# Performance work log

Hardware: AMD Instinct MI355X
Metric: run time of the kernel (lower is better)

Reference implementation:

```python
import jax, jax.numpy as jnp
import numpy as np

N_HEADS = 8
HEAD_DIM = 64


def setup_inputs() -> dict:
    key = jax.random.key(0)
    ks = jax.random.split(key, 5)
    B, L, D = 2, 2048, 512
    Dh = N_HEADS * HEAD_DIM  # 512
    scale_init = 0.02
    return {
        "x": jax.random.normal(ks[0], (B, L, D), dtype=jnp.float32),
        "wq": jax.random.normal(ks[1], (D, Dh), dtype=jnp.float32) * scale_init,
        "wk": jax.random.normal(ks[2], (D, Dh), dtype=jnp.float32) * scale_init,
        "wv": jax.random.normal(ks[3], (D, Dh), dtype=jnp.float32) * scale_init,
        "wo": jax.random.normal(ks[4], (Dh, D), dtype=jnp.float32) * scale_init,
    }


def reference(x, wq, wk, wv, wo):
    B, L, D = x.shape
    H, Dh = N_HEADS, HEAD_DIM
    scale = 1.0 / (Dh ** 0.5)

    q = (x @ wq).reshape(B, L, H, Dh)
    k = (x @ wk).reshape(B, L, H, Dh)
    v = (x @ wv).reshape(B, L, H, Dh)

    # [B, H, L, S] scores; diagonal (token attending to itself) is masked out.
    scores = jnp.einsum('blhe,bshe->bhls', q, k) * scale
    diag = jnp.eye(L, dtype=bool)  # [L, L]
    scores = jnp.where(diag, -jnp.inf, scores)
    attn = jax.nn.softmax(scores, axis=-1)

    out = jnp.einsum('bhls,bshd->blhd', attn, v).reshape(B, L, H * Dh)
    return out @ wo
```

## Files before the change

### kernel.cpp

```cpp
#include <hip/hip_runtime.h>
#include <hip/hip_bf16.h>
#include <math.h>

typedef __bf16 bf16;
typedef __bf16 bf16x8 __attribute__((ext_vector_type(8)));
typedef float f32x4 __attribute__((ext_vector_type(4)));

#define AS1 __attribute__((address_space(1)))
#define AS3 __attribute__((address_space(3)))

__device__ __forceinline__ void gload_lds16(const void* g, void* l) {
  __builtin_amdgcn_global_load_lds((const AS1 void*)g, (AS3 void*)l, 16, 0, 0);
}

__global__ __launch_bounds__(256) void cvt_x_kernel(const float* __restrict__ x,
                                                    bf16* __restrict__ xb) {
  int i = (blockIdx.x * 256 + threadIdx.x) * 8;
  float4 a = *(const float4*)(x + i);
  float4 b = *(const float4*)(x + i + 4);
  bf16x8 o;
  o[0] = (bf16)a.x; o[1] = (bf16)a.y; o[2] = (bf16)a.z; o[3] = (bf16)a.w;
  o[4] = (bf16)b.x; o[5] = (bf16)b.y; o[6] = (bf16)b.z; o[7] = (bf16)b.w;
  *(bf16x8*)(xb + i) = o;
}

__global__ __launch_bounds__(256) void transpose_w_kernel(
    const float* __restrict__ wq, const float* __restrict__ wk,
    const float* __restrict__ wv, const float* __restrict__ wo,
    bf16* __restrict__ wqkv_t, bf16* __restrict__ wo_t) {
  __shared__ float t[64 * 65];
  int ct = blockIdx.x & 31, kt = blockIdx.x >> 5;
  int p = ct >> 3;
  const float* src = (p == 0) ? wq : (p == 1) ? wk : (p == 2) ? wv : wo;
  int c0 = (ct & 7) * 64;
  int k0 = kt * 64;
  int tid = threadIdx.x;
  for (int i = 0; i < 16; ++i) {
    int idx = i * 256 + tid;
    int r = idx >> 6, c = idx & 63;
    t[r * 65 + c] = src[(size_t)(k0 + r) * 512 + c0 + c];
  }
  __syncthreads();
  for (int i = 0; i < 16; ++i) {
    int idx = i * 256 + tid;
    int cc = idx >> 6, kk = idx & 63;
    float v = t[kk * 65 + cc];
    int col = c0 + cc;
    if (p < 3) wqkv_t[(size_t)(p * 512 + col) * 512 + k0 + kk] = (bf16)v;
    else       wo_t[(size_t)col * 512 + k0 + kk] = (bf16)v;
  }
}

template <int MODE, int BM, int BN>
__global__ __launch_bounds__(256) void gemm_kernel(
    const bf16* __restrict__ A, const bf16* __restrict__ Bt,
    float* __restrict__ Cf, bf16* __restrict__ qw, bf16* __restrict__ kw,
    bf16* __restrict__ vtw, int M, int N, int K) {
  __shared__ bf16 ldsA[BM * 64];
  __shared__ bf16 ldsB[BN * 64];
  constexpr int MF = BM / 32;
  constexpr int NF = BN / 32;
  int tid = threadIdx.x;
  int wave = tid >> 6, l = tid & 63;
  int lr = l & 15, lg = l >> 4;
  int nbm = M / BM;
  int bm = blockIdx.x % nbm, bn = blockIdx.x / nbm;
  int wr = wave >> 1, wc = wave & 1;

  f32x4 acc[MF][NF] = {};

  for (int k0 = 0; k0 < K; k0 += 64) {
    #pragma unroll
    for (int i = 0; i < BM * 128 / 4096; ++i) {
      int off = i * 4096 + tid * 16;
      int r = off >> 7, cb = off & 127;
      gload_lds16((const char*)(A + (size_t)(bm * BM + r) * K + k0) + cb,
                  (char*)ldsA + i * 4096 + wave * 1024);
    }
    #pragma unroll
    for (int i = 0; i < BN * 128 / 4096; ++i) {
      int off = i * 4096 + tid * 16;
      int r = off >> 7, cb = off & 127;
      gload_lds16((const char*)(Bt + (size_t)(bn * BN + r) * K + k0) + cb,
                  (char*)ldsB + i * 4096 + wave * 1024);
    }
    __syncthreads();
    #pragma unroll
    for (int ks = 0; ks < 2; ++ks) {
      bf16x8 af[MF], bfr[NF];
      #pragma unroll
      for (int m = 0; m < MF; ++m)
        af[m] = *(const bf16x8*)(ldsA + (wr * (BM / 2) + m * 16 + lr) * 64 + ks * 32 + lg * 8);
      #pragma unroll
      for (int n = 0; n < NF; ++n)
        bfr[n] = *(const bf16x8*)(ldsB + (wc * (BN / 2) + n * 16 + lr) * 64 + ks * 32 + lg * 8);
      #pragma unroll
      for (int m = 0; m < MF; ++m)
        #pragma unroll
        for (int n = 0; n < NF; ++n)
          acc[m][n] = __builtin_amdgcn_mfma_f32_16x16x32_bf16(af[m], bfr[n], acc[m][n], 0, 0, 0);
    }
    __syncthreads();
  }

  #pragma unroll
  for (int m = 0; m < MF; ++m)
    #pragma unroll
    for (int n = 0; n < NF; ++n)
      #pragma unroll
      for (int j = 0; j < 4; ++j) {
        float v = acc[m][n][j];
        int row = bm * BM + wr * (BM / 2) + m * 16 + lg * 4 + j;
        int col = bn * BN + wc * (BN / 2) + n * 16 + lr;
        if (MODE == 1) {
          Cf[(size_t)row * N + col] = v;
        } else {
          int part = col >> 9, cp = col & 511;
          int h = cp >> 6, d = cp & 63;
          int b = row >> 11, lq = row & 2047;
          size_t bh = (size_t)(b * 8 + h);
          if (part == 0)      qw[(bh * 2048 + lq) * 64 + d] = (bf16)(v * 0.18033688f);
          else if (part == 1) kw[(bh * 2048 + lq) * 64 + d] = (bf16)v;
          else                vtw[(bh * 64 + d) * 2048 + lq] = (bf16)v;
        }
      }
}

__global__ __launch_bounds__(512) void attn_kernel(
    const bf16* __restrict__ qw, const bf16* __restrict__ kw,
    const bf16* __restrict__ vtw, bf16* __restrict__ pO0, bf16* __restrict__ pO1,
    float* __restrict__ pL0, float* __restrict__ pL1) {
  __shared__ bf16 ldsK[2][64 * 64];
  __shared__ bf16 ldsV[2][64 * 64];
  __shared__ bf16 ldsP[8][16 * 64];

  int swzb = ((blockIdx.x & 7) << 6) | (blockIdx.x >> 3);
  int qblk = swzb & 15, kv = (swzb >> 4) & 1, bh = swzb >> 5;

  int tid = threadIdx.x, wave = tid >> 6, l = tid & 63;
  int lr = l & 15, lg = l >> 4;
  const bf16* Q  = qw  + (size_t)bh * 2048 * 64;
  const bf16* Kp = kw  + (size_t)bh * 2048 * 64;
  const bf16* Vt = vtw + (size_t)bh * 64 * 2048;
  int q0 = qblk * 128;
  int td = qblk * 2 + (wave >> 2);
  int qrel = (wave & 3) * 16;

  bf16x8 qf[2];
  #pragma unroll
  for (int ks = 0; ks < 2; ++ks)
    qf[ks] = *(const bf16x8*)(Q + (size_t)(q0 + wave * 16 + lr) * 64 + ks * 32 + lg * 8);

  int rowT = tid >> 3;
  int colT = (tid * 16) & 127;
  int swzcol = colT ^ ((rowT & 7) << 4);
  int swzk = rowT * 128 + swzcol;
  size_t vsrc = (size_t)rowT * 4096 + swzcol;

  f32x4 acc_o[4] = {};
  float l_part[4] = {0.f, 0.f, 0.f, 0.f};

  auto stage = [&](int buf, int t) {
    gload_lds16((const char*)Kp + (size_t)t * 8192 + swzk, (char*)ldsK[buf] + wave * 1024);
    gload_lds16((const char*)Vt + (size_t)t * 128 + vsrc,  (char*)ldsV[buf] + wave * 1024);
  };

  int t0 = kv * 16;
  stage(0, t0);

  int rxor = (lr & 7) << 4;

  for (int tt = 0; tt < 16; ++tt) {
    int t = t0 + tt;
    int buf = tt & 1;
    if (tt < 15) {
      stage(buf ^ 1, t + 1);
      asm volatile("s_waitcnt vmcnt(2)" ::: "memory");
    } else {
      asm volatile("s_waitcnt vmcnt(0)" ::: "memory");
    }
    __builtin_amdgcn_s_barrier();
    __builtin_amdgcn_sched_barrier(0);

    f32x4 sa[4] = {};
    __builtin_amdgcn_s_setprio(1);
    #pragma unroll
    for (int ks = 0; ks < 2; ++ks) {
      #pragma unroll
      for (int n = 0; n < 4; ++n) {
        bf16x8 kf = *(const bf16x8*)((const char*)ldsK[buf] + (n * 16 + lr) * 128 +
                                     ((ks * 64 + lg * 16) ^ rxor));
        sa[n] = __builtin_amdgcn_mfma_f32_16x16x32_bf16(qf[ks], kf, sa[n], 0, 0, 0);
      }
    }
    __builtin_amdgcn_s_setprio(0);

    if (t == td) {
      #pragma unroll
      for (int n = 0; n < 4; ++n)
        #pragma unroll
        for (int j = 0; j < 4; ++j)
          if (n * 16 + lr == qrel + lg * 4 + j) sa[n][j] = -INFINITY;
    }

    #pragma unroll
    for (int n = 0; n < 4; ++n)
      #pragma unroll
      for (int j = 0; j < 4; ++j) {
        float p = exp2f(sa[n][j]);
        sa[n][j] = p;
        l_part[j] += p;
      }

    char* P = (char*)ldsP[wave];
    #pragma unroll
    for (int j = 0; j < 4; ++j) {
      int rowP = lg * 4 + j;
      #pragma unroll
      for (int n = 0; n < 4; ++n)
        *(bf16*)(P + rowP * 128 + (((n * 16 + lr) * 2) ^ ((rowP & 7) << 4))) = (bf16)sa[n][j];
    }

    __builtin_amdgcn_s_setprio(1);
    #pragma unroll
    for (int ks = 0; ks < 2; ++ks) {
      bf16x8 pf = *(const bf16x8*)(P + lr * 128 + ((ks * 64 + lg * 16) ^ rxor));
      #pragma unroll
      for (int n = 0; n < 4; ++n) {
        bf16x8 vf = *(const bf16x8*)((const char*)ldsV[buf] + (n * 16 + lr) * 128 +
                                     ((ks * 64 + lg * 16) ^ rxor));
        acc_o[n] = __builtin_amdgcn_mfma_f32_16x16x32_bf16(pf, vf, acc_o[n], 0, 0, 0);
      }
    }
    __builtin_amdgcn_s_setprio(0);
    __builtin_amdgcn_s_barrier();
  }

  #pragma unroll
  for (int j = 0; j < 4; ++j)
    #pragma unroll
    for (int dd = 1; dd < 16; dd <<= 1) l_part[j] += __shfl_xor(l_part[j], dd);

  bf16*  pO = kv ? pO1 : pO0;
  float* pL = kv ? pL1 : pL0;
  #pragma unroll
  for (int j = 0; j < 4; ++j) {
    int gq = q0 + wave * 16 + lg * 4 + j;
    if (lr == 0) pL[(size_t)bh * 2048 + gq] = l_part[j];
    #pragma unroll
    for (int n = 0; n < 4; ++n)
      pO[((size_t)bh * 2048 + gq) * 64 + n * 16 + lr] = (bf16)acc_o[n][j];
  }
}

__global__ __launch_bounds__(256) void combine_kernel(
    const bf16* __restrict__ pO0, const bf16* __restrict__ pO1,
    const float* __restrict__ pL0, const float* __restrict__ pL1,
    bf16* __restrict__ ao) {
  int idx = blockIdx.x * 256 + threadIdx.x;
  int e8 = idx * 8;
  int row = e8 >> 9, col = e8 & 511;
  int b = row >> 11, lq = row & 2047, h = col >> 6, d0 = col & 63;
  size_t bhq = (size_t)(b * 8 + h) * 2048 + lq;
  size_t src = bhq * 64 + d0;
  bf16x8 va = *(const bf16x8*)(pO0 + src);
  bf16x8 vb = *(const bf16x8*)(pO1 + src);
  float inv = 1.f / (pL0[bhq] + pL1[bhq]);
  bf16x8 o;
  #pragma unroll
  for (int i = 0; i < 8; ++i) o[i] = (bf16)(((float)va[i] + (float)vb[i]) * inv);
  *(bf16x8*)(ao + e8) = o;
}

extern "C" void kernel_launch(void* const* d_in, const int* in_sizes, int n_in,
                              void* d_out, int out_size, void* d_ws, size_t ws_size,
                              hipStream_t stream) {
  const float* x  = (const float*)d_in[0];
  const float* wq = (const float*)d_in[1];
  const float* wk = (const float*)d_in[2];
  const float* wv = (const float*)d_in[3];
  const float* wo = (const float*)d_in[4];

  if (ws_size < (24u << 20)) return;

  char* ws = (char*)d_ws;
  bf16* xb     = (bf16*)(ws);
  bf16* wqkv_t = (bf16*)(ws + (4 << 20));
  bf16* wo_t   = (bf16*)(ws + (6 << 20));
  bf16* q_ws   = (bf16*)(ws + (8 << 20));
  bf16* k_ws   = (bf16*)(ws + (12 << 20));
  bf16* vt_ws  = (bf16*)(ws + (16 << 20));
  bf16*  pO0 = (bf16*)(ws);
  float* pL0 = (float*)(ws + (4 << 20));
  float* pL1 = (float*)(ws + (4 << 20) + (128 << 10));
  bf16*  pO1 = (bf16*)(ws + (20 << 20));
  bf16*  ao  = (bf16*)(ws + (8 << 20));

  cvt_x_kernel<<<1024, 256, 0, stream>>>(x, xb);
  transpose_w_kernel<<<256, 256, 0, stream>>>(wq, wk, wv, wo, wqkv_t, wo_t);
  gemm_kernel<0, 64, 128><<<64 * 12, 256, 0, stream>>>(xb, wqkv_t, nullptr, q_ws, k_ws,
                                                       vt_ws, 4096, 1536, 512);
  attn_kernel<<<512, 512, 0, stream>>>(q_ws, k_ws, vt_ws, pO0, pO1, pL0, pL1);
  combine_kernel<<<1024, 256, 0, stream>>>(pO0, pO1, pL0, pL1, ao);
  gemm_kernel<1, 64, 64><<<64 * 8, 256, 0, stream>>>(ao, wo_t, (float*)d_out, nullptr,
                                                     nullptr, nullptr, 4096, 512, 512);
}
```

Before: 80.63 us.

## Double query rows per wave and split KV into four partitions

```diff
diff --git a/kernel.cpp b/kernel.cpp
--- a/kernel.cpp
+++ b/kernel.cpp
@@ -126,30 +126,36 @@
       }
 }
 
-__global__ __launch_bounds__(512) void attn_kernel(
+__global__ __launch_bounds__(512, 4) void attn_kernel(
     const bf16* __restrict__ qw, const bf16* __restrict__ kw,
-    const bf16* __restrict__ vtw, bf16* __restrict__ pO0, bf16* __restrict__ pO1,
-    float* __restrict__ pL0, float* __restrict__ pL1) {
+    const bf16* __restrict__ vtw,
+    bf16* __restrict__ pO0, bf16* __restrict__ pO1,
+    bf16* __restrict__ pO2, bf16* __restrict__ pO3,
+    float* __restrict__ pL0, float* __restrict__ pL1,
+    float* __restrict__ pL2, float* __restrict__ pL3) {
   __shared__ bf16 ldsK[2][64 * 64];
   __shared__ bf16 ldsV[2][64 * 64];
-  __shared__ bf16 ldsP[8][16 * 64];
+  __shared__ bf16 ldsP[8][2][16 * 64];
 
   int swzb = ((blockIdx.x & 7) << 6) | (blockIdx.x >> 3);
-  int qblk = swzb & 15, kv = (swzb >> 4) & 1, bh = swzb >> 5;
+  int qblk = swzb & 7, kv = (swzb >> 3) & 3, bh = swzb >> 5;
 
   int tid = threadIdx.x, wave = tid >> 6, l = tid & 63;
   int lr = l & 15, lg = l >> 4;
   const bf16* Q  = qw  + (size_t)bh * 2048 * 64;
   const bf16* Kp = kw  + (size_t)bh * 2048 * 64;
   const bf16* Vt = vtw + (size_t)bh * 64 * 2048;
-  int q0 = qblk * 128;
-  int td = qblk * 2 + (wave >> 2);
-  int qrel = (wave & 3) * 16;
-
-  bf16x8 qf[2];
-  #pragma unroll
-  for (int ks = 0; ks < 2; ++ks)
-    qf[ks] = *(const bf16x8*)(Q + (size_t)(q0 + wave * 16 + lr) * 64 + ks * 32 + lg * 8);
+  int q0 = qblk * 256;
+  int td = qblk * 4 + (wave >> 1);
+  int qrelA = (wave & 1) * 32;
+  int qrelB = qrelA + 16;
+
+  bf16x8 qfA[2], qfB[2];
+  #pragma unroll
+  for (int ks = 0; ks < 2; ++ks) {
+    qfA[ks] = *(const bf16x8*)(Q + (size_t)(q0 + wave * 32 + lr) * 64 + ks * 32 + lg * 8);
+    qfB[ks] = *(const bf16x8*)(Q + (size_t)(q0 + wave * 32 + 16 + lr) * 64 + ks * 32 + lg * 8);
+  }
 
   int rowT = tid >> 3;
   int colT = (tid * 16) & 127;
@@ -157,23 +163,23 @@
   int swzk = rowT * 128 + swzcol;
   size_t vsrc = (size_t)rowT * 4096 + swzcol;
 
-  f32x4 acc_o[4] = {};
-  float l_part[4] = {0.f, 0.f, 0.f, 0.f};
+  f32x4 accA[4] = {}, accB[4] = {};
+  float lA[4] = {0.f, 0.f, 0.f, 0.f}, lB[4] = {0.f, 0.f, 0.f, 0.f};
 
   auto stage = [&](int buf, int t) {
     gload_lds16((const char*)Kp + (size_t)t * 8192 + swzk, (char*)ldsK[buf] + wave * 1024);
     gload_lds16((const char*)Vt + (size_t)t * 128 + vsrc,  (char*)ldsV[buf] + wave * 1024);
   };
 
-  int t0 = kv * 16;
+  int t0 = kv * 8;
   stage(0, t0);
 
   int rxor = (lr & 7) << 4;
 
-  for (int tt = 0; tt < 16; ++tt) {
+  for (int tt = 0; tt < 8; ++tt) {
     int t = t0 + tt;
     int buf = tt & 1;
-    if (tt < 15) {
+    if (tt < 7) {
       stage(buf ^ 1, t + 1);
       asm volatile("s_waitcnt vmcnt(2)" ::: "memory");
     } else {
@@ -182,7 +188,7 @@
     __builtin_amdgcn_s_barrier();
     __builtin_amdgcn_sched_barrier(0);
 
-    f32x4 sa[4] = {};
+    f32x4 saA[4] = {}, saB[4] = {};
     __builtin_amdgcn_s_setprio(1);
     #pragma unroll
     for (int ks = 0; ks < 2; ++ks) {
@@ -190,7 +196,8 @@
       for (int n = 0; n < 4; ++n) {
         bf16x8 kf = *(const bf16x8*)((const char*)ldsK[buf] + (n * 16 + lr) * 128 +
                                      ((ks * 64 + lg * 16) ^ rxor));
-        sa[n] = __builtin_amdgcn_mfma_f32_16x16x32_bf16(qf[ks], kf, sa[n], 0, 0, 0);
+        saA[n] = __builtin_amdgcn_mfma_f32_16x16x32_bf16(qfA[ks], kf, saA[n], 0, 0, 0);
+        saB[n] = __builtin_amdgcn_mfma_f32_16x16x32_bf16(qfB[ks], kf, saB[n], 0, 0, 0);
       }
     }
     __builtin_amdgcn_s_setprio(0);
@@ -199,37 +206,39 @@
       #pragma unroll
       for (int n = 0; n < 4; ++n)
         #pragma unroll
-        for (int j = 0; j < 4; ++j)
-          if (n * 16 + lr == qrel + lg * 4 + j) sa[n][j] = -INFINITY;
-    }
-
+        for (int j = 0; j < 4; ++j) {
+          if (n * 16 + lr == qrelA + lg * 4 + j) saA[n][j] = -INFINITY;
+          if (n * 16 + lr == qrelB + lg * 4 + j) saB[n][j] = -INFINITY;
+        }
+    }
+
+    char* PA = (char*)ldsP[wave][0];
+    char* PB = (char*)ldsP[wave][1];
     #pragma unroll
     for (int n = 0; n < 4; ++n)
       #pragma unroll
       for (int j = 0; j < 4; ++j) {
-        float p = exp2f(sa[n][j]);
-        sa[n][j] = p;
-        l_part[j] += p;
+        int rowP = lg * 4 + j;
+        int cswz = ((n * 16 + lr) * 2) ^ ((rowP & 7) << 4);
+        float pA = exp2f(saA[n][j]);
+        lA[j] += pA;
+        *(bf16*)(PA + rowP * 128 + cswz) = (bf16)pA;
+        float pB = exp2f(saB[n][j]);
+        lB[j] += pB;
+        *(bf16*)(PB + rowP * 128 + cswz) = (bf16)pB;
       }
 
-    char* P = (char*)ldsP[wave];
-    #pragma unroll
-    for (int j = 0; j < 4; ++j) {
-      int rowP = lg * 4 + j;
-      #pragma unroll
-      for (int n = 0; n < 4; ++n)
-        *(bf16*)(P + rowP * 128 + (((n * 16 + lr) * 2) ^ ((rowP & 7) << 4))) = (bf16)sa[n][j];
-    }
-
     __builtin_amdgcn_s_setprio(1);
     #pragma unroll
     for (int ks = 0; ks < 2; ++ks) {
-      bf16x8 pf = *(const bf16x8*)(P + lr * 128 + ((ks * 64 + lg * 16) ^ rxor));
+      bf16x8 pfA = *(const bf16x8*)(PA + lr * 128 + ((ks * 64 + lg * 16) ^ rxor));
+      bf16x8 pfB = *(const bf16x8*)(PB + lr * 128 + ((ks * 64 + lg * 16) ^ rxor));
       #pragma unroll
       for (int n = 0; n < 4; ++n) {
         bf16x8 vf = *(const bf16x8*)((const char*)ldsV[buf] + (n * 16 + lr) * 128 +
                                      ((ks * 64 + lg * 16) ^ rxor));
-        acc_o[n] = __builtin_amdgcn_mfma_f32_16x16x32_bf16(pf, vf, acc_o[n], 0, 0, 0);
+        accA[n] = __builtin_amdgcn_mfma_f32_16x16x32_bf16(pfA, vf, accA[n], 0, 0, 0);
+        accB[n] = __builtin_amdgcn_mfma_f32_16x16x32_bf16(pfB, vf, accB[n], 0, 0, 0);
       }
     }
     __builtin_amdgcn_s_setprio(0);
@@ -239,23 +248,34 @@
   #pragma unroll
   for (int j = 0; j < 4; ++j)
     #pragma unroll
-    for (int dd = 1; dd < 16; dd <<= 1) l_part[j] += __shfl_xor(l_part[j], dd);
-
-  bf16*  pO = kv ? pO1 : pO0;
-  float* pL = kv ? pL1 : pL0;
+    for (int dd = 1; dd < 16; dd <<= 1) {
+      lA[j] += __shfl_xor(lA[j], dd);
+      lB[j] += __shfl_xor(lB[j], dd);
+    }
+
+  bf16*  pO = (kv == 0) ? pO0 : (kv == 1) ? pO1 : (kv == 2) ? pO2 : pO3;
+  float* pL = (kv == 0) ? pL0 : (kv == 1) ? pL1 : (kv == 2) ? pL2 : pL3;
   #pragma unroll
   for (int j = 0; j < 4; ++j) {
-    int gq = q0 + wave * 16 + lg * 4 + j;
-    if (lr == 0) pL[(size_t)bh * 2048 + gq] = l_part[j];
-    #pragma unroll
-    for (int n = 0; n < 4; ++n)
-      pO[((size_t)bh * 2048 + gq) * 64 + n * 16 + lr] = (bf16)acc_o[n][j];
+    int gqA = q0 + wave * 32 + lg * 4 + j;
+    int gqB = gqA + 16;
+    if (lr == 0) {
+      pL[(size_t)bh * 2048 + gqA] = lA[j];
+      pL[(size_t)bh * 2048 + gqB] = lB[j];
+    }
+    #pragma unroll
+    for (int n = 0; n < 4; ++n) {
+      pO[((size_t)bh * 2048 + gqA) * 64 + n * 16 + lr] = (bf16)accA[n][j];
+      pO[((size_t)bh * 2048 + gqB) * 64 + n * 16 + lr] = (bf16)accB[n][j];
+    }
   }
 }
 
 __global__ __launch_bounds__(256) void combine_kernel(
     const bf16* __restrict__ pO0, const bf16* __restrict__ pO1,
+    const bf16* __restrict__ pO2, const bf16* __restrict__ pO3,
     const float* __restrict__ pL0, const float* __restrict__ pL1,
+    const float* __restrict__ pL2, const float* __restrict__ pL3,
     bf16* __restrict__ ao) {
   int idx = blockIdx.x * 256 + threadIdx.x;
   int e8 = idx * 8;
@@ -263,12 +283,15 @@
   int b = row >> 11, lq = row & 2047, h = col >> 6, d0 = col & 63;
   size_t bhq = (size_t)(b * 8 + h) * 2048 + lq;
   size_t src = bhq * 64 + d0;
-  bf16x8 va = *(const bf16x8*)(pO0 + src);
-  bf16x8 vb = *(const bf16x8*)(pO1 + src);
-  float inv = 1.f / (pL0[bhq] + pL1[bhq]);
+  bf16x8 v0 = *(const bf16x8*)(pO0 + src);
+  bf16x8 v1 = *(const bf16x8*)(pO1 + src);
+  bf16x8 v2 = *(const bf16x8*)(pO2 + src);
+  bf16x8 v3 = *(const bf16x8*)(pO3 + src);
+  float inv = 1.f / (pL0[bhq] + pL1[bhq] + pL2[bhq] + pL3[bhq]);
   bf16x8 o;
   #pragma unroll
-  for (int i = 0; i < 8; ++i) o[i] = (bf16)(((float)va[i] + (float)vb[i]) * inv);
+  for (int i = 0; i < 8; ++i)
+    o[i] = (bf16)(((float)v0[i] + (float)v1[i] + (float)v2[i] + (float)v3[i]) * inv);
   *(bf16x8*)(ao + e8) = o;
 }
 
@@ -281,7 +304,7 @@
   const float* wv = (const float*)d_in[3];
   const float* wo = (const float*)d_in[4];
 
-  if (ws_size < (24u << 20)) return;
+  if (ws_size < (32u << 20)) return;
 
   char* ws = (char*)d_ws;
   bf16* xb     = (bf16*)(ws);
@@ -293,15 +316,20 @@
   bf16*  pO0 = (bf16*)(ws);
   float* pL0 = (float*)(ws + (4 << 20));
   float* pL1 = (float*)(ws + (4 << 20) + (128 << 10));
+  float* pL2 = (float*)(ws + (4 << 20) + (256 << 10));
+  float* pL3 = (float*)(ws + (4 << 20) + (384 << 10));
   bf16*  pO1 = (bf16*)(ws + (20 << 20));
+  bf16*  pO2 = (bf16*)(ws + (24 << 20));
+  bf16*  pO3 = (bf16*)(ws + (28 << 20));
   bf16*  ao  = (bf16*)(ws + (8 << 20));
 
   cvt_x_kernel<<<1024, 256, 0, stream>>>(x, xb);
   transpose_w_kernel<<<256, 256, 0, stream>>>(wq, wk, wv, wo, wqkv_t, wo_t);
   gemm_kernel<0, 64, 128><<<64 * 12, 256, 0, stream>>>(xb, wqkv_t, nullptr, q_ws, k_ws,
                                                        vt_ws, 4096, 1536, 512);
-  attn_kernel<<<512, 512, 0, stream>>>(q_ws, k_ws, vt_ws, pO0, pO1, pL0, pL1);
-  combine_kernel<<<1024, 256, 0, stream>>>(pO0, pO1, pL0, pL1, ao);
+  attn_kernel<<<512, 512, 0, stream>>>(q_ws, k_ws, vt_ws, pO0, pO1, pO2, pO3,
+                                       pL0, pL1, pL2, pL3);
+  combine_kernel<<<1024, 256, 0, stream>>>(pO0, pO1, pO2, pO3, pL0, pL1, pL2, pL3, ao);
   gemm_kernel<1, 64, 64><<<64 * 8, 256, 0, stream>>>(ao, wo_t, (float*)d_out, nullptr,
                                                      nullptr, nullptr, 4096, 512, 512);
 }
```

Result: no change. 82.22 us (+2.0%).
